# Performance work log

Hardware: AMD Instinct MI355X
Metric: run time of the kernel (lower is better)

The kernel has to match this reference:

```python
import jax, jax.numpy as jnp
import numpy as np

L, N, D_IN = 4, 2048, 1024
H, DH = 8, 64
INNER = H * DH          # 512
D_OUT = D_IN            # out_dim defaults to input_dim
SCALE = DH ** -0.5


def setup_inputs() -> dict:
    key = jax.random.key(0)
    ks = jax.random.split(key, 7)
    x = jax.random.normal(ks[0], (L, N, D_IN), jnp.float32)
    # torch Linear weights are [out_features, in_features]; xavier-ish scale
    Wq = jax.random.normal(ks[1], (INNER, D_IN), jnp.float32) * 0.03
    Wk = jax.random.normal(ks[2], (INNER, D_IN), jnp.float32) * 0.03
    Wv = jax.random.normal(ks[3], (INNER, D_IN), jnp.float32) * 0.03
    Wo = jax.random.normal(ks[4], (D_OUT, INNER), jnp.float32) * 0.03
    bo = jnp.zeros((D_OUT,), jnp.float32)
    # boolean key-padding mask [L, n]; ensure at least one valid key per row
    mask = jax.random.uniform(ks[5], (L, N)) < 0.9
    mask = mask.at[:, 0].set(True)
    return {"x": x, "Wq": Wq, "Wk": Wk, "Wv": Wv, "Wo": Wo, "bo": bo, "mask": mask}


def reference(x, Wq, Wk, Wv, Wo, bo, mask):
    # projections (Linear: y = x @ W^T), split heads: L n (h d) -> l h n d
    def split_heads(t):
        return t.reshape(L, N, H, DH).transpose(0, 2, 1, 3)

    q = split_heads(jnp.einsum('lnd,ed->lne', x, Wq))
    k = split_heads(jnp.einsum('lnd,ed->lne', x, Wk))  # context defaults to x
    v = split_heads(jnp.einsum('lnd,ed->lne', x, Wv))

    sim = jnp.einsum('lhnd,lhmd->lhnm', q, k) * SCALE   # [L,H,N,N]
    neg = -jnp.finfo(sim.dtype).max
    sim = jnp.where(mask[:, None, None, :], sim, neg)   # mask over key dim
    attn = jax.nn.softmax(sim, axis=-1)

    out = jnp.einsum('lhnm,lhmd->lhnd', attn, v)        # [L,H,N,DH]
    out = out.transpose(0, 2, 1, 3).reshape(L, N, INNER)
    return out @ Wo.T + bo                               # [L,N,D_OUT]
```

## Files before the change

### kernel.cpp

```cpp
#include <hip/hip_runtime.h>
#include <hip/hip_bf16.h>

#define L_DIM 4
#define N_DIM 2048
#define DIN   1024
#define H_DIM 8
#define DH    64
#define INNER 512

typedef __attribute__((ext_vector_type(8))) short short8;
typedef __attribute__((ext_vector_type(4))) float f32x4;

__device__ __forceinline__ unsigned short f2bf(float f) {
  unsigned u = __builtin_bit_cast(unsigned, f);
  u += 0x7fffu + ((u >> 16) & 1u);
  return (unsigned short)(u >> 16);
}

__device__ __forceinline__ unsigned cvtpk(float a, float b) {
  unsigned r;
  asm("v_cvt_pk_bf16_f32 %0, %1, %2" : "=v"(r) : "v"(a), "v"(b));
  return r;
}

__device__ __forceinline__ float fexp2(float x) {
  float r;
  asm("v_exp_f32 %0, %1" : "=v"(r) : "v"(x));
  return r;
}

typedef __attribute__((address_space(3))) unsigned int lds_uint;
typedef const __attribute__((address_space(1))) unsigned int glob_uint;
__device__ __forceinline__ void gl_lds16(const unsigned short* g,
                                         unsigned short* l) {
  __builtin_amdgcn_global_load_lds((glob_uint*)g, (lds_uint*)l, 16, 0, 0);
}

__global__ void cast_all(const float* __restrict__ x,
                         const float* __restrict__ wq,
                         const float* __restrict__ wk,
                         const float* __restrict__ wv,
                         const float* __restrict__ wo,
                         unsigned short* __restrict__ xb,
                         unsigned short* __restrict__ w3,
                         unsigned short* __restrict__ wob,
                         const unsigned char* __restrict__ mraw,
                         float* __restrict__ bias) {
  __shared__ int votes[2];
  int bid = blockIdx.x, t = threadIdx.x;
  if (bid == 10240) {
    if (t < 2) votes[t] = 0;
    __syncthreads();
    const unsigned int* m32 = (const unsigned int*)mraw;
    int anyf = 0, any8 = 0;
    for (int i = t; i < 2048; i += 256) {
      unsigned w = m32[i];
      if (w == 0x3f800000u) anyf = 1;
      if (w & 0xffffff00u) any8 = 1;
    }
    if (anyf) atomicOr(&votes[0], 1);
    if (any8) atomicOr(&votes[1], 1);
    __syncthreads();
    int fmt = votes[0] ? 2 : (votes[1] ? 1 : 0);
    for (int i = t; i < L_DIM * N_DIM; i += 256) {
      int mv;
      if (fmt == 2)      mv = ((const float*)mraw)[i] != 0.0f;
      else if (fmt == 1) mv = mraw[i] != 0;
      else               mv = ((const int*)mraw)[i] != 0;
      bias[i] = mv ? 0.0f : -1e30f;
    }
    return;
  }
  int i = (bid * 256 + t) * 4;
  const float* src; unsigned short* dst; int off;
  if (i < 8388608)      { src = x;  dst = xb;           off = i; }
  else if (i < 8912896) { src = wq; dst = w3;           off = i - 8388608; }
  else if (i < 9437184) { src = wk; dst = w3 + 524288;  off = i - 8912896; }
  else if (i < 9961472) { src = wv; dst = w3 + 1048576; off = i - 9437184; }
  else                  { src = wo; dst = wob;          off = i - 9961472; }
  float4 f = *(const float4*)(src + off);
  ushort4 o4;
  o4.x = f2bf(f.x); o4.y = f2bf(f.y); o4.z = f2bf(f.z); o4.w = f2bf(f.w);
  *(ushort4*)(dst + off) = o4;
}

__launch_bounds__(256, 3)
__global__ void gemm_qkv(const unsigned short* __restrict__ xb,
                         const unsigned short* __restrict__ w3,
                         unsigned short* __restrict__ qp,
                         unsigned short* __restrict__ kp,
                         unsigned short* __restrict__ vtp) {
  __shared__ __align__(16) unsigned short Sh[16384];
  const int tid = threadIdx.x, lane = tid & 63, wid = tid >> 6;
  const int l16 = lane & 15, quad = lane >> 4;
  const int wm = wid >> 1, wn = wid & 1;
  const int m0 = blockIdx.x * 128, n0 = blockIdx.y * 128;

  int aoff[2], boff[2], lofs[2];
#pragma unroll
  for (int it = 0; it < 2; ++it) {
    int c = it * 256 + wid * 64 + lane;
    int row = c >> 2, kseg = c & 3;
    aoff[it] = (m0 + row) * DIN + kseg * 8;
    boff[it] = (n0 + row) * DIN + kseg * 8;
    lofs[it] = (it * 256 + wid * 64) * 8;
  }

#pragma unroll
  for (int it = 0; it < 2; ++it) {
    gl_lds16(&xb[aoff[it]], &Sh[lofs[it]]);
    gl_lds16(&w3[boff[it]], &Sh[8192 + lofs[it]]);
  }

  f32x4 acc[4][4] = {};
  for (int t = 0; t < 32; ++t) {
    const int buf = t & 1;
    __syncthreads();
    if (t < 31) {
      int kt2 = (t + 1) * 32, b2 = buf ^ 1;
#pragma unroll
      for (int it = 0; it < 2; ++it) {
        gl_lds16(&xb[aoff[it] + kt2], &Sh[b2 * 4096 + lofs[it]]);
        gl_lds16(&w3[boff[it] + kt2], &Sh[8192 + b2 * 4096 + lofs[it]]);
      }
    }
    const unsigned short* As = &Sh[buf * 4096];
    const unsigned short* Bs = &Sh[8192 + buf * 4096];
    short8 af[4], bf[4];
#pragma unroll
    for (int mt = 0; mt < 4; ++mt)
      af[mt] = *(const short8*)&As[(wm * 64 + mt * 16 + l16) * 32 + quad * 8];
#pragma unroll
    for (int nt = 0; nt < 4; ++nt)
      bf[nt] = *(const short8*)&Bs[(wn * 64 + nt * 16 + l16) * 32 + quad * 8];
#pragma unroll
    for (int mt = 0; mt < 4; ++mt)
#pragma unroll
      for (int nt = 0; nt < 4; ++nt)
        acc[mt][nt] = __builtin_amdgcn_mfma_f32_16x16x32_bf16(
            af[mt], bf[nt], acc[mt][nt], 0, 0, 0);
  }
  if (blockIdx.y >= 8) {
    const int l = m0 >> 11, mloc = m0 & 2047;
#pragma unroll
    for (int chunk = 0; chunk < 2; ++chunk) {
      __syncthreads();
      if (wn == chunk) {
#pragma unroll
        for (int mt = 0; mt < 4; ++mt)
#pragma unroll
          for (int nt = 0; nt < 4; ++nt) {
            int col = nt * 16 + l16;
            int rowb = wm * 64 + mt * 16 + quad * 4;
            ushort4 pv;
            pv.x = f2bf(acc[mt][nt][0]);
            pv.y = f2bf(acc[mt][nt][1]);
            pv.z = f2bf(acc[mt][nt][2]);
            pv.w = f2bf(acc[mt][nt][3]);
            *(ushort4*)&Sh[col * 136 + rowb] = pv;
          }
      }
      __syncthreads();
      int hh = ((n0 + chunk * 64) & 511) >> 6;
#pragma unroll
      for (int it = 0; it < 4; ++it) {
        int c = it * 256 + tid;
        int cl = c >> 4, seg = c & 15;
        short8 vv = *(const short8*)&Sh[cl * 136 + seg * 8];
        *(short8*)&vtp[((size_t)((l * H_DIM + hh) * DH + cl)) * N_DIM + mloc +
                       seg * 8] = vv;
      }
    }
  } else {
    const int l = m0 >> 11, nloc = m0 & 2047;
    const int hbase = (n0 & 511) >> 6;
    unsigned short* dstp = (n0 >> 9) ? kp : qp;
#pragma unroll
    for (int chunk = 0; chunk < 2; ++chunk) {
      __syncthreads();
      if (wn == chunk) {
#pragma unroll
        for (int mt = 0; mt < 4; ++mt)
#pragma unroll
          for (int nt = 0; nt < 4; ++nt) {
            int col = nt * 16 + l16;
            int rowb = wm * 64 + mt * 16 + quad * 4;
#pragma unroll
            for (int r = 0; r < 4; ++r)
              Sh[(rowb + r) * 72 + col] = f2bf(acc[mt][nt][r]);
          }
      }
      __syncthreads();
      int hh = hbase + chunk;
      unsigned short* db =
          dstp + ((size_t)(l * H_DIM + hh) * N_DIM + nloc) * DH;
#pragma unroll
      for (int it = 0; it < 4; ++it) {
        int c = it * 256 + tid;
        int row = c >> 3, seg = c & 7;
        short8 vv = *(const short8*)&Sh[row * 72 + seg * 8];
        *(short8*)&db[row * DH + seg * 8] = vv;
      }
    }
  }
}

#define KVB 32
#define PW_S 32
__launch_bounds__(128, 4)
__global__ void attn_kernel(const unsigned short* __restrict__ qg,
                            const unsigned short* __restrict__ kg,
                            const unsigned short* __restrict__ vtg,
                            const float* __restrict__ bias,
                            unsigned short* __restrict__ aout) {
  __shared__ __align__(16) unsigned short Ks[2][KVB * 64];
  __shared__ __align__(16) unsigned short Vs[2][64 * KVB];
  __shared__ __align__(16) unsigned short Pw[32 * PW_S];
  const int tid = threadIdx.x, lane = tid & 63, wid = tid >> 6;
  const int l16 = lane & 15, quad = lane >> 4;
  const int bid = blockIdx.x;
  const int xcd = bid & 7, j = bid >> 3;
  const int lh = xcd * 4 + (j >> 6);
  const int q0 = (j & 63) << 5;
  const int l = lh >> 3, h = lh & 7;
  const unsigned short* Qb = qg + (size_t)lh * N_DIM * DH;
  const unsigned short* Kb = kg + (size_t)lh * N_DIM * DH;
  const unsigned short* Vt = vtg + (size_t)lh * DH * N_DIM;
  const float* bl = bias + l * N_DIM;

  short8 qf[2];
#pragma unroll
  for (int ks = 0; ks < 2; ++ks)
    qf[ks] = *(const short8*)&Qb[(q0 + wid * 16 + l16) * DH + ks * 32 +
                                 quad * 8];

  f32x4 o[4] = {};
  float lsum = 0.f;

  int kof[2], vof0[2], ldsb[2];
  size_t vof[2];
#pragma unroll
  for (int it = 0; it < 2; ++it) {
    int c = it * 128 + wid * 64 + lane;
    int key = c >> 3, sl = c & 7, gs = (sl + key) & 7;
    kof[it] = key * DH + gs * 8;
    int d = c >> 2, sv = c & 3, gv = (sv + d) & 3;
    vof[it] = (size_t)d * N_DIM + gv * 8;
    ldsb[it] = c * 8;
  }
  (void)vof0;

#pragma unroll
  for (int it = 0; it < 2; ++it) {
    gl_lds16(&Kb[kof[it]], &Ks[0][ldsb[it]]);
    gl_lds16(&Vt[vof[it]], &Vs[0][ldsb[it]]);
  }

  for (int t = 0; t < 64; ++t) {
    const int kv = t << 5, buf = t & 1;
    __syncthreads();
    if (t < 63) {
      int kv2 = kv + KVB, b2 = buf ^ 1;
#pragma unroll
      for (int it = 0; it < 2; ++it) {
        gl_lds16(&Kb[(kv2 << 6) + kof[it]], &Ks[b2][ldsb[it]]);
        gl_lds16(&Vt[vof[it] + kv2], &Vs[b2][ldsb[it]]);
      }
    }
    const unsigned short* Kst = Ks[buf];
    const unsigned short* Vst = Vs[buf];

    f32x4 sc[2] = {};
#pragma unroll
    for (int nt = 0; nt < 2; ++nt)
#pragma unroll
      for (int ks = 0; ks < 2; ++ks) {
        int s = (ks * 4 + quad - l16) & 7;
        short8 kf = *(const short8*)&Kst[(nt * 16 + l16) * 64 + s * 8];
        sc[nt] = __builtin_amdgcn_mfma_f32_16x16x32_bf16(kf, qf[ks], sc[nt],
                                                         0, 0, 0);
      }
    unsigned short* pr = &Pw[(wid * 16 + l16) * PW_S];
#pragma unroll
    for (int nt = 0; nt < 2; ++nt) {
      float4 b4 = *(const float4*)&bl[kv + nt * 16 + quad * 4];
      float p0 = fexp2(fmaf(sc[nt][0], 0.18033688011f, b4.x));
      float p1 = fexp2(fmaf(sc[nt][1], 0.18033688011f, b4.y));
      float p2 = fexp2(fmaf(sc[nt][2], 0.18033688011f, b4.z));
      float p3 = fexp2(fmaf(sc[nt][3], 0.18033688011f, b4.w));
      lsum += (p0 + p1) + (p2 + p3);
      uint2 pkv = make_uint2(cvtpk(p0, p1), cvtpk(p2, p3));
      int gk = nt * 2 + (quad >> 1);
      int s = (gk + l16) & 3;
      *(uint2*)&pr[s * 8 + (quad & 1) * 4] = pkv;
    }
    {
      int sp = (quad + l16) & 3;
      short8 pa = *(const short8*)&Pw[(wid * 16 + l16) * PW_S + sp * 8];
#pragma unroll
      for (int nt = 0; nt < 4; ++nt) {
        int dd = nt * 16 + l16;
        int sv2 = (quad - l16) & 3;
        short8 vb = *(const short8*)&Vst[dd * KVB + sv2 * 8];
        o[nt] = __builtin_amdgcn_mfma_f32_16x16x32_bf16(pa, vb, o[nt],
                                                        0, 0, 0);
      }
    }
  }
  lsum += __shfl_xor(lsum, 16);
  lsum += __shfl_xor(lsum, 32);
#pragma unroll
  for (int r = 0; r < 4; ++r) {
    float inv = 1.f / __shfl(lsum, quad * 4 + r);
    int row = q0 + wid * 16 + quad * 4 + r;
#pragma unroll
    for (int nt = 0; nt < 4; ++nt)
      aout[(size_t)(l * N_DIM + row) * INNER + h * DH + nt * 16 + l16] =
          f2bf(o[nt][r] * inv);
  }
}

__launch_bounds__(256, 4)
__global__ void gemm_out(const unsigned short* __restrict__ a,
                         const unsigned short* __restrict__ wo,
                         const float* __restrict__ bo,
                         float* __restrict__ out) {
  __shared__ __align__(16) unsigned short Sh[12288];
  const int tid = threadIdx.x, lane = tid & 63, wid = tid >> 6;
  const int l16 = lane & 15, quad = lane >> 4;
  const int wm = wid >> 1, wn = wid & 1;
  const int m0 = blockIdx.x * 128, n0 = blockIdx.y * 64;

  int aoff[2], lofsA[2];
#pragma unroll
  for (int it = 0; it < 2; ++it) {
    int c = it * 256 + wid * 64 + lane;
    int row = c >> 2, kseg = c & 3;
    aoff[it] = (m0 + row) * INNER + kseg * 8;
    lofsA[it] = (it * 256 + wid * 64) * 8;
  }
  int boff, lofsB;
  {
    int c = wid * 64 + lane;
    int row = c >> 2, kseg = c & 3;
    boff = (n0 + row) * INNER + kseg * 8;
    lofsB = (wid * 64) * 8;
  }

#pragma unroll
  for (int it = 0; it < 2; ++it)
    gl_lds16(&a[aoff[it]], &Sh[lofsA[it]]);
  gl_lds16(&wo[boff], &Sh[8192 + lofsB]);

  f32x4 acc[4][2] = {};
  for (int t = 0; t < 16; ++t) {
    const int buf = t & 1;
    __syncthreads();
    if (t < 15) {
      int kt2 = (t + 1) * 32, b2 = buf ^ 1;
#pragma unroll
      for (int it = 0; it < 2; ++it)
        gl_lds16(&a[aoff[it] + kt2], &Sh[b2 * 4096 + lofsA[it]]);
      gl_lds16(&wo[boff + kt2], &Sh[8192 + b2 * 2048 + lofsB]);
    }
    const unsigned short* As = &Sh[buf * 4096];
    const unsigned short* Bs = &Sh[8192 + buf * 2048];
    short8 af[4], bf[2];
#pragma unroll
    for (int mt = 0; mt < 4; ++mt)
      af[mt] = *(const short8*)&As[(wm * 64 + mt * 16 + l16) * 32 + quad * 8];
#pragma unroll
    for (int nt = 0; nt < 2; ++nt)
      bf[nt] = *(const short8*)&Bs[(wn * 32 + nt * 16 + l16) * 32 + quad * 8];
#pragma unroll
    for (int mt = 0; mt < 4; ++mt)
#pragma unroll
      for (int nt = 0; nt < 2; ++nt)
        acc[mt][nt] = __builtin_amdgcn_mfma_f32_16x16x32_bf16(
            af[mt], bf[nt], acc[mt][nt], 0, 0, 0);
  }
#pragma unroll
  for (int mt = 0; mt < 4; ++mt)
#pragma unroll
    for (int nt = 0; nt < 2; ++nt)
#pragma unroll
      for (int r = 0; r < 4; ++r) {
        int grow = m0 + wm * 64 + mt * 16 + quad * 4 + r;
        int gcol = n0 + wn * 32 + nt * 16 + l16;
        out[(size_t)grow * DIN + gcol] = acc[mt][nt][r] + bo[gcol];
      }
}

extern "C" void kernel_launch(void* const* d_in, const int* in_sizes, int n_in,
                              void* d_out, int out_size, void* d_ws,
                              size_t ws_size, hipStream_t stream) {
  const float* x  = (const float*)d_in[0];
  const float* Wq = (const float*)d_in[1];
  const float* Wk = (const float*)d_in[2];
  const float* Wv = (const float*)d_in[3];
  const float* Wo = (const float*)d_in[4];
  const float* bo = (const float*)d_in[5];
  const unsigned char* mask = (const unsigned char*)d_in[6];
  float* out = (float*)d_out;

  char* ws = (char*)d_ws;
  unsigned short* xb  = (unsigned short*)(ws + 0);
  unsigned short* w3  = (unsigned short*)(ws + 16777216);
  unsigned short* wob = (unsigned short*)(ws + 19922944);
  unsigned short* q   = (unsigned short*)(ws + 20971520);
  unsigned short* k   = (unsigned short*)(ws + 29360128);
  unsigned short* vt  = (unsigned short*)(ws + 37748736);
  unsigned short* att = (unsigned short*)(ws + 46137344);
  float* bias         = (float*)(ws + 54525952);

  cast_all<<<10241, 256, 0, stream>>>(x, Wq, Wk, Wv, Wo, xb, w3, wob, mask,
                                      bias);
  gemm_qkv<<<dim3(64, 12), 256, 0, stream>>>(xb, w3, q, k, vt);
  attn_kernel<<<2048, 128, 0, stream>>>(q, k, vt, bias, att);
  gemm_out<<<dim3(64, 16), 256, 0, stream>>>(att, wob, bo, out);
}
```

Baseline: 225.2 us.

## Enlarge attention tiles to 64 queries and 64-key blocks with 4 waves

```diff
diff --git a/kernel.cpp b/kernel.cpp
--- a/kernel.cpp
+++ b/kernel.cpp
@@ -205,23 +205,22 @@
   }
 }
 
-#define KVB 32
-#define PW_S 32
-__launch_bounds__(128, 4)
+#define PW_S 64
+__launch_bounds__(256, 4)
 __global__ void attn_kernel(const unsigned short* __restrict__ qg,
                             const unsigned short* __restrict__ kg,
                             const unsigned short* __restrict__ vtg,
                             const float* __restrict__ bias,
                             unsigned short* __restrict__ aout) {
-  __shared__ __align__(16) unsigned short Ks[2][KVB * 64];
-  __shared__ __align__(16) unsigned short Vs[2][64 * KVB];
-  __shared__ __align__(16) unsigned short Pw[32 * PW_S];
+  __shared__ __align__(16) unsigned short Ks[2][64 * 64];
+  __shared__ __align__(16) unsigned short Vs[2][64 * 64];
+  __shared__ __align__(16) unsigned short Pw[64 * PW_S];
   const int tid = threadIdx.x, lane = tid & 63, wid = tid >> 6;
   const int l16 = lane & 15, quad = lane >> 4;
   const int bid = blockIdx.x;
   const int xcd = bid & 7, j = bid >> 3;
-  const int lh = xcd * 4 + (j >> 6);
-  const int q0 = (j & 63) << 5;
+  const int lh = xcd * 4 + (j >> 5);
+  const int q0 = (j & 31) << 6;
   const int l = lh >> 3, h = lh & 7;
   const unsigned short* Qb = qg + (size_t)lh * N_DIM * DH;
   const unsigned short* Kb = kg + (size_t)lh * N_DIM * DH;
@@ -237,18 +236,16 @@
   f32x4 o[4] = {};
   float lsum = 0.f;
 
-  int kof[2], vof0[2], ldsb[2];
+  int kof[2], ldsb[2];
   size_t vof[2];
 #pragma unroll
   for (int it = 0; it < 2; ++it) {
-    int c = it * 128 + wid * 64 + lane;
-    int key = c >> 3, sl = c & 7, gs = (sl + key) & 7;
-    kof[it] = key * DH + gs * 8;
-    int d = c >> 2, sv = c & 3, gv = (sv + d) & 3;
-    vof[it] = (size_t)d * N_DIM + gv * 8;
-    ldsb[it] = c * 8;
-  }
-  (void)vof0;
+    int c = it * 256 + tid;
+    int rr = c >> 3, sl = c & 7, gs = (sl + rr) & 7;
+    kof[it] = rr * DH + gs * 8;
+    vof[it] = (size_t)rr * N_DIM + gs * 8;
+    ldsb[it] = (it * 256 + wid * 64) * 8;
+  }
 
 #pragma unroll
   for (int it = 0; it < 2; ++it) {
@@ -256,11 +253,11 @@
     gl_lds16(&Vt[vof[it]], &Vs[0][ldsb[it]]);
   }
 
-  for (int t = 0; t < 64; ++t) {
-    const int kv = t << 5, buf = t & 1;
+  for (int t = 0; t < 32; ++t) {
+    const int kv = t << 6, buf = t & 1;
     __syncthreads();
-    if (t < 63) {
-      int kv2 = kv + KVB, b2 = buf ^ 1;
+    if (t < 31) {
+      int kv2 = kv + 64, b2 = buf ^ 1;
 #pragma unroll
       for (int it = 0; it < 2; ++it) {
         gl_lds16(&Kb[(kv2 << 6) + kof[it]], &Ks[b2][ldsb[it]]);
@@ -270,9 +267,9 @@
     const unsigned short* Kst = Ks[buf];
     const unsigned short* Vst = Vs[buf];
 
-    f32x4 sc[2] = {};
-#pragma unroll
-    for (int nt = 0; nt < 2; ++nt)
+    f32x4 sc[4] = {};
+#pragma unroll
+    for (int nt = 0; nt < 4; ++nt)
 #pragma unroll
       for (int ks = 0; ks < 2; ++ks) {
         int s = (ks * 4 + quad - l16) & 7;
@@ -282,7 +279,7 @@
       }
     unsigned short* pr = &Pw[(wid * 16 + l16) * PW_S];
 #pragma unroll
-    for (int nt = 0; nt < 2; ++nt) {
+    for (int nt = 0; nt < 4; ++nt) {
       float4 b4 = *(const float4*)&bl[kv + nt * 16 + quad * 4];
       float p0 = fexp2(fmaf(sc[nt][0], 0.18033688011f, b4.x));
       float p1 = fexp2(fmaf(sc[nt][1], 0.18033688011f, b4.y));
@@ -291,17 +288,18 @@
       lsum += (p0 + p1) + (p2 + p3);
       uint2 pkv = make_uint2(cvtpk(p0, p1), cvtpk(p2, p3));
       int gk = nt * 2 + (quad >> 1);
-      int s = (gk + l16) & 3;
+      int s = (gk + l16) & 7;
       *(uint2*)&pr[s * 8 + (quad & 1) * 4] = pkv;
     }
-    {
-      int sp = (quad + l16) & 3;
+#pragma unroll
+    for (int g = 0; g < 2; ++g) {
+      int sp = (g * 4 + quad + l16) & 7;
       short8 pa = *(const short8*)&Pw[(wid * 16 + l16) * PW_S + sp * 8];
 #pragma unroll
       for (int nt = 0; nt < 4; ++nt) {
         int dd = nt * 16 + l16;
-        int sv2 = (quad - l16) & 3;
-        short8 vb = *(const short8*)&Vst[dd * KVB + sv2 * 8];
+        int sv2 = (g * 4 + quad - l16) & 7;
+        short8 vb = *(const short8*)&Vst[dd * 64 + sv2 * 8];
         o[nt] = __builtin_amdgcn_mfma_f32_16x16x32_bf16(pa, vb, o[nt],
                                                         0, 0, 0);
       }
@@ -416,6 +414,6 @@
   cast_all<<<10241, 256, 0, stream>>>(x, Wq, Wk, Wv, Wo, xb, w3, wob, mask,
                                       bias);
   gemm_qkv<<<dim3(64, 12), 256, 0, stream>>>(xb, w3, q, k, vt);
-  attn_kernel<<<2048, 128, 0, stream>>>(q, k, vt, bias, att);
+  attn_kernel<<<1024, 256, 0, stream>>>(q, k, vt, bias, att);
   gemm_out<<<dim3(64, 16), 256, 0, stream>>>(att, wob, bo, out);
 }
```

Measured after the change: 210.5 us. 1.07x faster.
